# Performance work log

Hardware: AMD Instinct MI355X
Metric: run time of the kernel (lower is better)

Reference implementation:

```python
import jax, jax.numpy as jnp
import numpy as np

N = 50000      # nodes
E = 200000     # edges
S = 8          # edge feature dim
F_IN = 32      # node feature dim after GraphMasking
F = 32         # ECCConv channels
G = 512        # graphs in disjoint batch
P = 1024       # preference pairs
N_OUT = 1      # config['n_out']


def _ecc(x, e, src, tgt, Wk, bk, root, b):
    # edge-conditioned filters: [E, F_in, F_out]
    kern = (e @ Wk + bk).reshape(E, x.shape[1], -1)
    # gather source node feats, apply per-edge filter, scatter-sum to targets
    msgs = jnp.einsum('ei,eio->eo', x[src], kern)
    agg = jax.ops.segment_sum(msgs, tgt, num_segments=N)
    return jax.nn.relu(agg + x @ root + b)


def setup_inputs() -> dict:
    key = jax.random.key(0)
    ks = jax.random.split(key, 12)
    s = 0.1
    return {
        'x': jax.random.normal(ks[0], (N, F_IN + 1), jnp.float32),
        'e': jax.random.normal(ks[1], (E, S), jnp.float32),
        'sources': jax.random.randint(ks[2], (E,), 0, N),
        'targets': jax.random.randint(ks[3], (E,), 0, N),
        'seg': jnp.sort(jax.random.randint(ks[4], (N,), 0, G)),
        'idx_a': jax.random.randint(ks[5], (P,), 0, G),
        'idx_b': jax.random.randint(ks[6], (P,), 0, G),
        'Wk1': jax.random.normal(ks[7], (S, F_IN * F), jnp.float32) * s,
        'bk1': jnp.zeros((F_IN * F,), jnp.float32),
        'root1': jax.random.normal(ks[8], (F_IN, F), jnp.float32) * s,
        'b1': jnp.zeros((F,), jnp.float32),
        'Wk2': jax.random.normal(ks[9], (S, F * F), jnp.float32) * s,
        'bk2': jnp.zeros((F * F,), jnp.float32),
        'root2': jax.random.normal(ks[10], (F, F), jnp.float32) * s,
        'b2': jnp.zeros((F,), jnp.float32),
        'Wd': jax.random.normal(ks[11], (F, N_OUT), jnp.float32) * s,
        'bd': jnp.zeros((N_OUT,), jnp.float32),
    }


def reference(x, e, sources, targets, seg, idx_a, idx_b,
              Wk1, bk1, root1, b1, Wk2, bk2, root2, b2, Wd, bd):
    h = x[:, :-1]                         # GraphMasking: drop mask column
    h = _ecc(h, e, sources, targets, Wk1, bk1, root1, b1)
    h = _ecc(h, e, sources, targets, Wk2, bk2, root2, b2)
    # tf.cast(x, int32): truncation (exact for nonneg relu output),
    # non-differentiable like the original cast.
    h = jax.lax.stop_gradient(jnp.trunc(h))
    pooled = jax.ops.segment_sum(h, seg, num_segments=G)   # GlobalSumPool
    out = jax.nn.relu(pooled @ Wd + bd)                    # Dense(n_out, relu)
    return out[idx_b] - out[idx_a]                         # pref lookup diff
```

## Files before the change

kernel.cpp:

```cpp
#include <hip/hip_runtime.h>

#define N_NODES 50000
#define N_EDGES 200000
#define S_DIM   8
#define F_DIM   32
#define G_SEG   512
#define P_PAIRS 1024
#define A_COLS  288
#define SCAN_B  196

__global__ __launch_bounds__(256)
void zero_init(int* __restrict__ deg, float* __restrict__ pooled)
{
    const int gid = blockIdx.x * 256 + threadIdx.x;
    if (gid < N_NODES) deg[gid] = 0;
    if (gid < G_SEG * F_DIM) pooled[gid] = 0.f;
}

__global__ __launch_bounds__(256)
void deg_hist(const int* __restrict__ src, int* __restrict__ deg)
{
    const int e = blockIdx.x * 256 + threadIdx.x;
    if (e < N_EDGES) atomicAdd(&deg[src[e]], 1);
}

__global__ __launch_bounds__(256)
void sum_blocks(const int* __restrict__ deg, int* __restrict__ partial)
{
    __shared__ int sd[256];
    const int t = threadIdx.x;
    const int n = blockIdx.x * 256 + t;
    sd[t] = (n < N_NODES) ? deg[n] : 0;
    __syncthreads();
    for (int off = 128; off > 0; off >>= 1) {
        if (t < off) sd[t] += sd[t + off];
        __syncthreads();
    }
    if (t == 0) partial[blockIdx.x] = sd[0];
}

__global__ __launch_bounds__(256)
void scan_partials(const int* __restrict__ partial, int* __restrict__ blockoff)
{
    __shared__ int sd[256];
    const int t = threadIdx.x;
    sd[t] = (t < SCAN_B) ? partial[t] : 0;
    __syncthreads();
    for (int off = 1; off < 256; off <<= 1) {
        int v = (t >= off) ? sd[t - off] : 0;
        __syncthreads();
        sd[t] += v;
        __syncthreads();
    }
    if (t < SCAN_B) blockoff[t] = (t == 0) ? 0 : sd[t - 1];
}

__global__ __launch_bounds__(256)
void write_rowstart(const int* __restrict__ deg, const int* __restrict__ blockoff,
                    int* __restrict__ rowstart, int* __restrict__ cursor)
{
    __shared__ int sd[256];
    const int t = threadIdx.x;
    const int n = blockIdx.x * 256 + t;
    const int d = (n < N_NODES) ? deg[n] : 0;
    sd[t] = d;
    __syncthreads();
    for (int off = 1; off < 256; off <<= 1) {
        int v = (t >= off) ? sd[t - off] : 0;
        __syncthreads();
        sd[t] += v;
        __syncthreads();
    }
    if (n < N_NODES) {
        const int rs = blockoff[blockIdx.x] + sd[t] - d;
        rowstart[n] = rs;
        cursor[n]   = rs;
    }
    if (blockIdx.x == 0 && t == 0) rowstart[N_NODES] = N_EDGES;
}

__global__ __launch_bounds__(256)
void csr_scatter(const int* __restrict__ src, const int* __restrict__ tgt,
                 int* __restrict__ cursor, int* __restrict__ eid,
                 int* __restrict__ srcs, int* __restrict__ tgts)
{
    const int e = blockIdx.x * 256 + threadIdx.x;
    if (e < N_EDGES) {
        const int sn  = src[e];
        const int pos = atomicAdd(&cursor[sn], 1);
        eid[pos]  = e;
        srcs[pos] = sn;
        tgts[pos] = tgt[e];
    }
}

template <int LAYER>
__global__ __launch_bounds__(320)
void node_gemm(const float* __restrict__ hsrc,
               const float* __restrict__ Wk, const float* __restrict__ bk,
               const float* __restrict__ root, const float* __restrict__ bias,
               float* __restrict__ A, float* __restrict__ agg)
{
    const int NB = 64;
    __shared__ float hh[NB][F_DIM];

    const int nb   = blockIdx.x * NB;
    const int nmax = (N_NODES - nb < NB) ? (N_NODES - nb) : NB;

    if (LAYER == 0) {
        for (int idx = threadIdx.x; idx < nmax * F_DIM; idx += 320) {
            const int n = idx >> 5, i = idx & 31;
            hh[n][i] = hsrc[(size_t)(nb + n) * (F_DIM + 1) + i];
        }
    } else {
        const float4* src4 = (const float4*)(hsrc + (size_t)nb * F_DIM);
        for (int idx = threadIdx.x; idx < nmax * (F_DIM / 4); idx += 320) {
            float4 v = src4[idx];
            v.x = v.x > 0.f ? v.x : 0.f;
            v.y = v.y > 0.f ? v.y : 0.f;
            v.z = v.z > 0.f ? v.z : 0.f;
            v.w = v.w > 0.f ? v.w : 0.f;
            ((float4*)hh)[idx] = v;
        }
    }
    __syncthreads();

    const int c = threadIdx.x;
    float w[F_DIM];
    float init = 0.f;
    if (c < 256) {
        const int s = c >> 5, o = c & 31;
        #pragma unroll
        for (int i = 0; i < F_DIM; ++i) w[i] = Wk[s * (F_DIM * F_DIM) + i * F_DIM + o];
    } else if (c < A_COLS) {
        const int o = c & 31;
        #pragma unroll
        for (int i = 0; i < F_DIM; ++i) w[i] = bk[i * F_DIM + o];
    } else {
        const int o = c - A_COLS;
        #pragma unroll
        for (int i = 0; i < F_DIM; ++i) w[i] = root[i * F_DIM + o];
        init = bias[o];
    }

    for (int n = 0; n < nmax; ++n) {
        const float4* hv = (const float4*)hh[n];
        float acc = init;
        #pragma unroll
        for (int i4 = 0; i4 < F_DIM / 4; ++i4) {
            float4 h4 = hv[i4];
            acc += h4.x * w[4*i4]   + h4.y * w[4*i4+1]
                 + h4.z * w[4*i4+2] + h4.w * w[4*i4+3];
        }
        if (c < A_COLS) A[(size_t)(nb + n) * A_COLS + c] = acc;
        else            agg[(size_t)(nb + n) * F_DIM + (c - A_COLS)] = acc;
    }
}

__global__ __launch_bounds__(256)
void edge_msg(const float* __restrict__ A, const float* __restrict__ evec,
              const int* __restrict__ eid, const int* __restrict__ srcs,
              const int* __restrict__ tgts, float* __restrict__ agg)
{
    const int gid = blockIdx.x * 256 + threadIdx.x;
    const int i   = gid >> 5;
    const int o   = gid & 31;
    if (i >= N_EDGES) return;

    const int e  = eid[i];
    const int sn = srcs[i];
    const int tn = tgts[i];
    const float* Ap = A + (size_t)sn * A_COLS + o;
    const float* ev = evec + (size_t)e * S_DIM;

    float msg = Ap[8 * F_DIM];
    #pragma unroll
    for (int s = 0; s < S_DIM; ++s)
        msg += ev[s] * Ap[s * F_DIM];

    atomicAdd(&agg[(size_t)tn * F_DIM + o], msg);
}

__global__ __launch_bounds__(256)
void pool_kernel(const float* __restrict__ agg2, const int* __restrict__ seg,
                 float* __restrict__ pooled)
{
    const int o    = threadIdx.x & 31;
    const int r    = threadIdx.x >> 5;
    const int base = blockIdx.x * 256 + r * 32;

    int   curseg = -1;
    float acc    = 0.f;
    for (int i = 0; i < 32; ++i) {
        const int n = base + i;
        if (n >= N_NODES) break;
        const int sg = seg[n];
        if (sg != curseg) {
            if (curseg >= 0 && acc != 0.f)
                atomicAdd(&pooled[(size_t)curseg * F_DIM + o], acc);
            curseg = sg;
            acc = 0.f;
        }
        float v = agg2[(size_t)n * F_DIM + o];
        v = v > 0.f ? v : 0.f;
        acc += truncf(v);
    }
    if (curseg >= 0 && acc != 0.f)
        atomicAdd(&pooled[(size_t)curseg * F_DIM + o], acc);
}

__global__ __launch_bounds__(512)
void head_kernel(const float* __restrict__ pooled, const float* __restrict__ Wd,
                 const float* __restrict__ bd, const int* __restrict__ ia,
                 const int* __restrict__ ib, float* __restrict__ out)
{
    __shared__ float og[G_SEG];
    const int g = threadIdx.x;
    if (g < G_SEG) {
        float acc = bd[0];
        #pragma unroll
        for (int i = 0; i < F_DIM; ++i) acc += pooled[(size_t)g * F_DIM + i] * Wd[i];
        og[g] = acc > 0.f ? acc : 0.f;
    }
    __syncthreads();
    for (int p = threadIdx.x; p < P_PAIRS; p += 512)
        out[p] = og[ib[p]] - og[ia[p]];
}

extern "C" void kernel_launch(void* const* d_in, const int* in_sizes, int n_in,
                              void* d_out, int out_size, void* d_ws, size_t ws_size,
                              hipStream_t stream)
{
    const float* x    = (const float*)d_in[0];
    const float* e    = (const float*)d_in[1];
    const int*   src  = (const int*)d_in[2];
    const int*   tgt  = (const int*)d_in[3];
    const int*   seg  = (const int*)d_in[4];
    const int*   ia   = (const int*)d_in[5];
    const int*   ib   = (const int*)d_in[6];
    const float* Wk1  = (const float*)d_in[7];
    const float* bk1  = (const float*)d_in[8];
    const float* root1= (const float*)d_in[9];
    const float* b1   = (const float*)d_in[10];
    const float* Wk2  = (const float*)d_in[11];
    const float* bk2  = (const float*)d_in[12];
    const float* root2= (const float*)d_in[13];
    const float* b2   = (const float*)d_in[14];
    const float* Wd   = (const float*)d_in[15];
    const float* bd   = (const float*)d_in[16];
    float* out = (float*)d_out;

    float* A      = (float*)d_ws;
    float* ag1    = A   + (size_t)N_NODES * A_COLS;
    float* ag2    = ag1 + (size_t)N_NODES * F_DIM;
    float* pooled = ag2 + (size_t)N_NODES * F_DIM;
    int*   deg      = (int*)(pooled + (size_t)G_SEG * F_DIM);
    int*   cursor   = deg + N_NODES;
    int*   rowstart = cursor + N_NODES;
    int*   partial  = rowstart + (N_NODES + 1);
    int*   blockoff = partial + SCAN_B;
    int*   eid      = blockoff + SCAN_B;
    int*   srcs     = eid + N_EDGES;
    int*   tgts     = srcs + N_EDGES;

    const int nblk = (N_NODES + 63) / 64;
    const int eblk = (N_EDGES + 255) / 256;
    const int mblk = (N_EDGES * 32) / 256;

    zero_init     <<<SCAN_B, 256, 0, stream>>>(deg, pooled);
    deg_hist      <<<eblk, 256, 0, stream>>>(src, deg);
    sum_blocks    <<<SCAN_B, 256, 0, stream>>>(deg, partial);
    scan_partials <<<1, 256, 0, stream>>>(partial, blockoff);
    write_rowstart<<<SCAN_B, 256, 0, stream>>>(deg, blockoff, rowstart, cursor);
    csr_scatter   <<<eblk, 256, 0, stream>>>(src, tgt, cursor, eid, srcs, tgts);

    node_gemm<0><<<nblk, 320, 0, stream>>>(x,   Wk1, bk1, root1, b1, A, ag1);
    edge_msg    <<<mblk, 256, 0, stream>>>(A, e, eid, srcs, tgts, ag1);
    node_gemm<1><<<nblk, 320, 0, stream>>>(ag1, Wk2, bk2, root2, b2, A, ag2);
    edge_msg    <<<mblk, 256, 0, stream>>>(A, e, eid, srcs, tgts, ag2);

    pool_kernel<<<SCAN_B, 256, 0, stream>>>(ag2, seg, pooled);
    head_kernel<<<1, 512, 0, stream>>>(pooled, Wd, bd, ia, ib, out);
}
```

Measured before the change: 178.8 us.

## Fuse per-node filter GEMM with edge messages in shared memory, pre-sort edge features

```diff
diff --git a/kernel.cpp b/kernel.cpp
--- a/kernel.cpp
+++ b/kernel.cpp
@@ -8,6 +8,7 @@
 #define P_PAIRS 1024
 #define A_COLS  288
 #define SCAN_B  196
+#define NB      32
 
 __global__ __launch_bounds__(256)
 void zero_init(int* __restrict__ deg, float* __restrict__ pooled)
@@ -81,28 +82,62 @@
 
 __global__ __launch_bounds__(256)
 void csr_scatter(const int* __restrict__ src, const int* __restrict__ tgt,
-                 int* __restrict__ cursor, int* __restrict__ eid,
-                 int* __restrict__ srcs, int* __restrict__ tgts)
+                 const float* __restrict__ evec, int* __restrict__ cursor,
+                 int* __restrict__ srcs, int* __restrict__ tgts,
+                 float* __restrict__ esort)
 {
     const int e = blockIdx.x * 256 + threadIdx.x;
     if (e < N_EDGES) {
         const int sn  = src[e];
         const int pos = atomicAdd(&cursor[sn], 1);
-        eid[pos]  = e;
         srcs[pos] = sn;
         tgts[pos] = tgt[e];
-    }
+        const float4* s4 = (const float4*)(evec + (size_t)e * S_DIM);
+        float4* d4 = (float4*)(esort + (size_t)pos * S_DIM);
+        d4[0] = s4[0];
+        d4[1] = s4[1];
+    }
+}
+
+template <int LAYER>
+__global__ __launch_bounds__(256)
+void agg_init(const float* __restrict__ hsrc, const float* __restrict__ root,
+              const float* __restrict__ bias, float* __restrict__ agg)
+{
+    __shared__ float r[F_DIM * F_DIM];
+    __shared__ float bsh[F_DIM];
+    for (int t = threadIdx.x; t < F_DIM * F_DIM; t += 256) r[t] = root[t];
+    if (threadIdx.x < F_DIM) bsh[threadIdx.x] = bias[threadIdx.x];
+    __syncthreads();
+
+    const int gid = blockIdx.x * 256 + threadIdx.x;
+    if (gid >= N_NODES * F_DIM) return;
+    const int n = gid >> 5, o = gid & 31;
+
+    float acc = bsh[o];
+    #pragma unroll
+    for (int i = 0; i < F_DIM; ++i) {
+        float h;
+        if (LAYER == 0) h = hsrc[(size_t)n * (F_DIM + 1) + i];
+        else {
+            h = hsrc[(size_t)n * F_DIM + i];
+            h = h > 0.f ? h : 0.f;
+        }
+        acc += h * r[i * F_DIM + o];
+    }
+    agg[gid] = acc;
 }
 
 template <int LAYER>
 __global__ __launch_bounds__(320)
-void node_gemm(const float* __restrict__ hsrc,
+void fused_ecc(const float* __restrict__ hsrc,
                const float* __restrict__ Wk, const float* __restrict__ bk,
-               const float* __restrict__ root, const float* __restrict__ bias,
-               float* __restrict__ A, float* __restrict__ agg)
-{
-    const int NB = 64;
+               const int* __restrict__ rowstart, const int* __restrict__ srcs,
+               const int* __restrict__ tgts, const float* __restrict__ esort,
+               float* __restrict__ agg)
+{
     __shared__ float hh[NB][F_DIM];
+    __shared__ float At[NB][A_COLS];
 
     const int nb   = blockIdx.x * NB;
     const int nmax = (N_NODES - nb < NB) ? (N_NODES - nb) : NB;
@@ -113,9 +148,9 @@
             hh[n][i] = hsrc[(size_t)(nb + n) * (F_DIM + 1) + i];
         }
     } else {
-        const float4* src4 = (const float4*)(hsrc + (size_t)nb * F_DIM);
+        const float4* s4 = (const float4*)(hsrc + (size_t)nb * F_DIM);
         for (int idx = threadIdx.x; idx < nmax * (F_DIM / 4); idx += 320) {
-            float4 v = src4[idx];
+            float4 v = s4[idx];
             v.x = v.x > 0.f ? v.x : 0.f;
             v.y = v.y > 0.f ? v.y : 0.f;
             v.z = v.z > 0.f ? v.z : 0.f;
@@ -126,59 +161,47 @@
     __syncthreads();
 
     const int c = threadIdx.x;
-    float w[F_DIM];
-    float init = 0.f;
-    if (c < 256) {
-        const int s = c >> 5, o = c & 31;
+    if (c < A_COLS) {
+        float w[F_DIM];
+        const int o = c & 31;
+        if (c < 256) {
+            const int s = c >> 5;
+            #pragma unroll
+            for (int i = 0; i < F_DIM; ++i) w[i] = Wk[s * (F_DIM * F_DIM) + i * F_DIM + o];
+        } else {
+            #pragma unroll
+            for (int i = 0; i < F_DIM; ++i) w[i] = bk[i * F_DIM + o];
+        }
+        for (int n = 0; n < nmax; ++n) {
+            const float4* hv = (const float4*)hh[n];
+            float acc = 0.f;
+            #pragma unroll
+            for (int i4 = 0; i4 < F_DIM / 4; ++i4) {
+                float4 h4 = hv[i4];
+                acc += h4.x * w[4*i4]   + h4.y * w[4*i4+1]
+                     + h4.z * w[4*i4+2] + h4.w * w[4*i4+3];
+            }
+            At[n][c] = acc;
+        }
+    }
+    __syncthreads();
+
+    const int r0 = rowstart[nb];
+    const int r1 = rowstart[nb + nmax];
+    const int nwork = (r1 - r0) * F_DIM;
+    for (int idx = threadIdx.x; idx < nwork; idx += 320) {
+        const int pos = r0 + (idx >> 5);
+        const int o   = idx & 31;
+        const int ls  = srcs[pos] - nb;
+        const int tn  = tgts[pos];
+        const float* ev = esort + (size_t)pos * S_DIM;
+        const float* Ar = At[ls];
+        float m = Ar[8 * F_DIM + o];
         #pragma unroll
-        for (int i = 0; i < F_DIM; ++i) w[i] = Wk[s * (F_DIM * F_DIM) + i * F_DIM + o];
-    } else if (c < A_COLS) {
-        const int o = c & 31;
-        #pragma unroll
-        for (int i = 0; i < F_DIM; ++i) w[i] = bk[i * F_DIM + o];
-    } else {
-        const int o = c - A_COLS;
-        #pragma unroll
-        for (int i = 0; i < F_DIM; ++i) w[i] = root[i * F_DIM + o];
-        init = bias[o];
-    }
-
-    for (int n = 0; n < nmax; ++n) {
-        const float4* hv = (const float4*)hh[n];
-        float acc = init;
-        #pragma unroll
-        for (int i4 = 0; i4 < F_DIM / 4; ++i4) {
-            float4 h4 = hv[i4];
-            acc += h4.x * w[4*i4]   + h4.y * w[4*i4+1]
-                 + h4.z * w[4*i4+2] + h4.w * w[4*i4+3];
-        }
-        if (c < A_COLS) A[(size_t)(nb + n) * A_COLS + c] = acc;
-        else            agg[(size_t)(nb + n) * F_DIM + (c - A_COLS)] = acc;
-    }
-}
-
-__global__ __launch_bounds__(256)
-void edge_msg(const float* __restrict__ A, const float* __restrict__ evec,
-              const int* __restrict__ eid, const int* __restrict__ srcs,
-              const int* __restrict__ tgts, float* __restrict__ agg)
-{
-    const int gid = blockIdx.x * 256 + threadIdx.x;
-    const int i   = gid >> 5;
-    const int o   = gid & 31;
-    if (i >= N_EDGES) return;
-
-    const int e  = eid[i];
-    const int sn = srcs[i];
-    const int tn = tgts[i];
-    const float* Ap = A + (size_t)sn * A_COLS + o;
-    const float* ev = evec + (size_t)e * S_DIM;
-
-    float msg = Ap[8 * F_DIM];
-    #pragma unroll
-    for (int s = 0; s < S_DIM; ++s)
-        msg += ev[s] * Ap[s * F_DIM];
-
-    atomicAdd(&agg[(size_t)tn * F_DIM + o], msg);
+        for (int s = 0; s < S_DIM; ++s)
+            m += ev[s] * Ar[s * F_DIM + o];
+        atomicAdd(&agg[(size_t)tn * F_DIM + o], m);
+    }
 }
 
 __global__ __launch_bounds__(256)
@@ -250,34 +273,33 @@
     const float* bd   = (const float*)d_in[16];
     float* out = (float*)d_out;
 
-    float* A      = (float*)d_ws;
-    float* ag1    = A   + (size_t)N_NODES * A_COLS;
+    float* ag1    = (float*)d_ws;
     float* ag2    = ag1 + (size_t)N_NODES * F_DIM;
     float* pooled = ag2 + (size_t)N_NODES * F_DIM;
-    int*   deg      = (int*)(pooled + (size_t)G_SEG * F_DIM);
+    float* esort  = pooled + (size_t)G_SEG * F_DIM;
+    int*   deg      = (int*)(esort + (size_t)N_EDGES * S_DIM);
     int*   cursor   = deg + N_NODES;
     int*   rowstart = cursor + N_NODES;
     int*   partial  = rowstart + (N_NODES + 1);
     int*   blockoff = partial + SCAN_B;
-    int*   eid      = blockoff + SCAN_B;
-    int*   srcs     = eid + N_EDGES;
+    int*   srcs     = blockoff + SCAN_B;
     int*   tgts     = srcs + N_EDGES;
 
-    const int nblk = (N_NODES + 63) / 64;
     const int eblk = (N_EDGES + 255) / 256;
-    const int mblk = (N_EDGES * 32) / 256;
+    const int fblk = (N_NODES + NB - 1) / NB;
+    const int iblk = (N_NODES * F_DIM + 255) / 256;
 
     zero_init     <<<SCAN_B, 256, 0, stream>>>(deg, pooled);
     deg_hist      <<<eblk, 256, 0, stream>>>(src, deg);
     sum_blocks    <<<SCAN_B, 256, 0, stream>>>(deg, partial);
     scan_partials <<<1, 256, 0, stream>>>(partial, blockoff);
     write_rowstart<<<SCAN_B, 256, 0, stream>>>(deg, blockoff, rowstart, cursor);
-    csr_scatter   <<<eblk, 256, 0, stream>>>(src, tgt, cursor, eid, srcs, tgts);
-
-    node_gemm<0><<<nblk, 320, 0, stream>>>(x,   Wk1, bk1, root1, b1, A, ag1);
-    edge_msg    <<<mblk, 256, 0, stream>>>(A, e, eid, srcs, tgts, ag1);
-    node_gemm<1><<<nblk, 320, 0, stream>>>(ag1, Wk2, bk2, root2, b2, A, ag2);
-    edge_msg    <<<mblk, 256, 0, stream>>>(A, e, eid, srcs, tgts, ag2);
+    csr_scatter   <<<eblk, 256, 0, stream>>>(src, tgt, e, cursor, srcs, tgts, esort);
+
+    agg_init<0><<<iblk, 256, 0, stream>>>(x, root1, b1, ag1);
+    fused_ecc<0><<<fblk, 320, 0, stream>>>(x,   Wk1, bk1, rowstart, srcs, tgts, esort, ag1);
+    agg_init<1><<<iblk, 256, 0, stream>>>(ag1, root2, b2, ag2);
+    fused_ecc<1><<<fblk, 320, 0, stream>>>(ag1, Wk2, bk2, rowstart, srcs, tgts, esort, ag2);
 
     pool_kernel<<<SCAN_B, 256, 0, stream>>>(ag2, seg, pooled);
     head_kernel<<<1, 512, 0, stream>>>(pooled, Wd, bd, ia, ib, out);
```

Result: slower. 204.4 us (+14.3%).
